# Kernel optimization log

Hardware: AMD Instinct MI355X
Metric: run time of the kernel (lower is better)

## Reference

```python
import jax, jax.numpy as jnp
import numpy as np

H = 32          # hidden_size
L = 10          # linear_size
EPS = 1e-14


def _lstm_cell(x, h, c, Wih, Whh, bih, bhh):
    # torch LSTMCell: gates ordered [i, f, g, o]
    gates = x @ Wih.T + bih + h @ Whh.T + bhh
    i, f, g, o = jnp.split(gates, 4, axis=-1)
    i = jax.nn.sigmoid(i)
    f = jax.nn.sigmoid(f)
    g = jnp.tanh(g)
    o = jax.nn.sigmoid(o)
    c_new = f * c + i * g
    h_new = o * jnp.tanh(c_new)
    return h_new, c_new


def setup_inputs() -> dict:
    key = jax.random.key(0)
    ks = jax.random.split(key, 24)
    B, N = 8, 100000
    inp = {
        "x": jax.random.normal(ks[0], (B, N), jnp.float32),
        "grad": jax.random.normal(ks[1], (B, N), jnp.float32),
        "h0": jax.random.normal(ks[2], (B, N, H), jnp.float32),
        "c0": jax.random.normal(ks[3], (B, N, H), jnp.float32),
        "h1": jax.random.normal(ks[4], (B, N, H), jnp.float32),
        "c1": jax.random.normal(ks[5], (B, N, H), jnp.float32),
        # initial_transform: Linear(2, L) -> tanh -> Linear(L, L)
        "W1": jax.random.normal(ks[6], (L, 2), jnp.float32) * 0.3,
        "b1": jax.random.normal(ks[7], (L,), jnp.float32) * 0.1,
        "W2": jax.random.normal(ks[8], (L, L), jnp.float32) * 0.3,
        "b2": jax.random.normal(ks[9], (L,), jnp.float32) * 0.1,
        # LSTMCell layer 0 (input L) and layer 1 (input H)
        "Wih0": jax.random.normal(ks[10], (4 * H, L), jnp.float32) * 0.1,
        "Whh0": jax.random.normal(ks[11], (4 * H, H), jnp.float32) * 0.1,
        "bih0": jax.random.normal(ks[12], (4 * H,), jnp.float32) * 0.1,
        "bhh0": jax.random.normal(ks[13], (4 * H,), jnp.float32) * 0.1,
        "Wih1": jax.random.normal(ks[14], (4 * H, H), jnp.float32) * 0.1,
        "Whh1": jax.random.normal(ks[15], (4 * H, H), jnp.float32) * 0.1,
        "bih1": jax.random.normal(ks[16], (4 * H,), jnp.float32) * 0.1,
        "bhh1": jax.random.normal(ks[17], (4 * H,), jnp.float32) * 0.1,
        # fc: Linear(H, 1)
        "Wfc": jax.random.normal(ks[18], (1, H), jnp.float32) * 0.1,
        "bfc": jax.random.normal(ks[19], (1,), jnp.float32) * 0.1,
    }
    return inp


def reference(x, grad, h0, c0, h1, c1, W1, b1, W2, b2,
              Wih0, Whh0, bih0, bhh0, Wih1, Whh1, bih1, bhh1, Wfc, bfc):
    B, N = x.shape
    BN = B * N
    g = grad.reshape(BN, 1)
    # gradient preprocessing: [sign, log(|g| + eps)]
    inp = jnp.concatenate([jnp.sign(g), jnp.log(jnp.abs(g) + EPS)], axis=1)  # (BN, 2)
    t = jnp.tanh(inp @ W1.T + b1) @ W2.T + b2                                # (BN, L)
    # batched across all n variables simultaneously (no cross-variable recurrence)
    h0n, c0n = _lstm_cell(t, h0.reshape(BN, H), c0.reshape(BN, H), Wih0, Whh0, bih0, bhh0)
    h1n, c1n = _lstm_cell(h0n, h1.reshape(BN, H), c1.reshape(BN, H), Wih1, Whh1, bih1, bhh1)
    delta = (h1n @ Wfc.T + bfc).reshape(B, N)
    x_new = x + delta
    return (x_new,
            h0n.reshape(B, N, H), c0n.reshape(B, N, H),
            h1n.reshape(B, N, H), c1n.reshape(B, N, H),
            delta)
```

## Files before the change

### kernel.cpp

```cpp
#include <hip/hip_runtime.h>


typedef __attribute__((ext_vector_type(8))) short bf16x8;
typedef __attribute__((ext_vector_type(4))) float f32x4;

#define HH 32
#define LL 10
#define NG 128

__device__ __forceinline__ short f2bf(float x) {
  __bf16 b = (__bf16)x;
  return __builtin_bit_cast(short, b);
}
__device__ __forceinline__ float fsig(float x) {
  return __builtin_amdgcn_rcpf(1.0f + __expf(-x));
}
__device__ __forceinline__ float ftanh(float x) {
  return fmaf(2.0f, __builtin_amdgcn_rcpf(1.0f + __expf(-2.0f * x)), -1.0f);
}

__global__ __launch_bounds__(256, 3) void l2o_fused(
    const float* __restrict__ x, const float* __restrict__ grad,
    const float* __restrict__ h0, const float* __restrict__ c0,
    const float* __restrict__ h1, const float* __restrict__ c1,
    const float* __restrict__ W1, const float* __restrict__ b1,
    const float* __restrict__ W2, const float* __restrict__ b2,
    const float* __restrict__ Wih0, const float* __restrict__ Whh0,
    const float* __restrict__ bih0, const float* __restrict__ bhh0,
    const float* __restrict__ Wih1, const float* __restrict__ Whh1,
    const float* __restrict__ bih1, const float* __restrict__ bhh1,
    const float* __restrict__ Wfc, const float* __restrict__ bfc,
    float* __restrict__ out, int BNi)
{
  const size_t BN = (size_t)BNi;
  float* __restrict__ xout  = out;
  float* __restrict__ h0out = out + BN;
  float* __restrict__ c0out = out + BN + BN * HH;
  float* __restrict__ h1out = out + BN + 2 * BN * HH;
  float* __restrict__ c1out = out + BN + 3 * BN * HH;
  float* __restrict__ dout  = out + BN + 4 * BN * HH;

  __shared__ __align__(16) short wih0L[2][NG][8];
  __shared__ __align__(16) short whh0L[4][NG][8];
  __shared__ __align__(16) short wih1L[4][NG][8];
  __shared__ __align__(16) short whh1L[4][NG][8];
  __shared__ __align__(16) short tsg0[4][64][8];
  __shared__ __align__(4)  short tsg1[4][64][2];
  __shared__ __align__(16) short hsg[4][4][16][8];

  const int tid = threadIdx.x;
  for (int idx = tid; idx < NG * HH; idx += 256) {
    int n = idx >> 5, k = idx & 31;
    whh0L[k >> 3][n][k & 7] = f2bf(Whh0[n * HH + k]);
    wih1L[k >> 3][n][k & 7] = f2bf(Wih1[n * HH + k]);
    whh1L[k >> 3][n][k & 7] = f2bf(Whh1[n * HH + k]);
  }
  for (int idx = tid; idx < NG * 16; idx += 256) {
    int n = idx >> 4, k = idx & 15;
    wih0L[k >> 3][n][k & 7] = (k < LL) ? f2bf(Wih0[n * LL + k]) : (short)0;
  }

  const int lane = tid & 63;
  const int w = tid >> 6;
  const int col = lane & 15;
  const int g = lane >> 4;

  float biasv0[8], biasv1[8];
#pragma unroll
  for (int nt = 0; nt < 8; ++nt) {
    biasv0[nt] = bih0[nt * 16 + col] + bhh0[nt * 16 + col];
    biasv1[nt] = bih1[nt * 16 + col] + bhh1[nt * 16 + col];
  }
  const float wfc0 = Wfc[col], wfc1 = Wfc[16 + col];
  const float bfcv = bfc[0];

  const int ebase = blockIdx.x * 256 + w * 64;

  {
    float gv = grad[ebase + lane];
    float sg = (gv > 0.f) ? 1.f : ((gv < 0.f) ? -1.f : 0.f);
    float lg = __logf(fabsf(gv) + 1e-14f);
    float u[LL], t[LL];
#pragma unroll
    for (int j = 0; j < LL; ++j)
      u[j] = ftanh(W1[2 * j] * sg + W1[2 * j + 1] * lg + b1[j]);
#pragma unroll
    for (int j = 0; j < LL; ++j) {
      float a = b2[j];
#pragma unroll
      for (int k = 0; k < LL; ++k) a += W2[j * LL + k] * u[k];
      t[j] = a;
    }
    bf16x8 tv0;
#pragma unroll
    for (int s = 0; s < 8; ++s) tv0[s] = f2bf(t[s]);
    *reinterpret_cast<bf16x8*>(&tsg0[w][lane][0]) = tv0;
    tsg1[w][lane][0] = f2bf(t[8]);
    tsg1[w][lane][1] = f2bf(t[9]);
  }
  __syncthreads();

#pragma unroll 1
  for (int st = 0; st < 4; ++st) {
    const int m16 = ebase + st * 16;
    const int mrow = 4 * g;

    bf16x8 a_t = {0, 0, 0, 0, 0, 0, 0, 0};
    if (g == 0) a_t = *reinterpret_cast<const bf16x8*>(&tsg0[w][st * 16 + col][0]);
    else if (g == 1) {
      a_t[0] = tsg1[w][st * 16 + col][0];
      a_t[1] = tsg1[w][st * 16 + col][1];
    }
    const float4* hp = reinterpret_cast<const float4*>(h0 + (size_t)(m16 + col) * HH + 8 * g);
    float4 v0 = hp[0], v1 = hp[1];
    bf16x8 a_h0;
    a_h0[0] = f2bf(v0.x); a_h0[1] = f2bf(v0.y); a_h0[2] = f2bf(v0.z); a_h0[3] = f2bf(v0.w);
    a_h0[4] = f2bf(v1.x); a_h0[5] = f2bf(v1.y); a_h0[6] = f2bf(v1.z); a_h0[7] = f2bf(v1.w);

    float c0r[2][4];
#pragma unroll
    for (int kk = 0; kk < 2; ++kk)
#pragma unroll
      for (int r = 0; r < 4; ++r)
        c0r[kk][r] = c0[(size_t)(m16 + mrow + r) * HH + kk * 16 + col];

    f32x4 acc[8];
#pragma unroll
    for (int nt = 0; nt < 8; ++nt) {
      float bv = biasv0[nt];
      f32x4 a = {bv, bv, bv, bv};
      acc[nt] = a;
    }
#pragma unroll
    for (int nt = 0; nt < 8; ++nt) {
      bf16x8 bih = {0, 0, 0, 0, 0, 0, 0, 0};
      if (g < 2) bih = *reinterpret_cast<const bf16x8*>(&wih0L[g][nt * 16 + col][0]);
      acc[nt] = __builtin_amdgcn_mfma_f32_16x16x32_bf16(a_t, bih, acc[nt], 0, 0, 0);
      bf16x8 bhh = *reinterpret_cast<const bf16x8*>(&whh0L[g][nt * 16 + col][0]);
      acc[nt] = __builtin_amdgcn_mfma_f32_16x16x32_bf16(a_h0, bhh, acc[nt], 0, 0, 0);
    }

    const float4* h1p = reinterpret_cast<const float4*>(h1 + (size_t)(m16 + col) * HH + 8 * g);
    float4 w0 = h1p[0], w1v = h1p[1];

#pragma unroll
    for (int kk = 0; kk < 2; ++kk) {
      const int k = kk * 16 + col;
#pragma unroll
      for (int r = 0; r < 4; ++r) {
        const size_t e2 = (size_t)(m16 + mrow + r);
        float iv = fsig(acc[0 + kk][r]);
        float fv = fsig(acc[2 + kk][r]);
        float gv = ftanh(acc[4 + kk][r]);
        float ov = fsig(acc[6 + kk][r]);
        float cn = fv * c0r[kk][r] + iv * gv;
        float hn = ov * ftanh(cn);
        c0out[e2 * HH + k] = cn;
        h0out[e2 * HH + k] = hn;
        hsg[w][k >> 3][mrow + r][k & 7] = f2bf(hn);
      }
    }
    asm volatile("s_waitcnt lgkmcnt(0)" ::: "memory");

    bf16x8 a_hn = *reinterpret_cast<const bf16x8*>(&hsg[w][g][col][0]);
    bf16x8 a_h1;
    a_h1[0] = f2bf(w0.x);  a_h1[1] = f2bf(w0.y);  a_h1[2] = f2bf(w0.z);  a_h1[3] = f2bf(w0.w);
    a_h1[4] = f2bf(w1v.x); a_h1[5] = f2bf(w1v.y); a_h1[6] = f2bf(w1v.z); a_h1[7] = f2bf(w1v.w);

    float c1r[2][4];
#pragma unroll
    for (int kk = 0; kk < 2; ++kk)
#pragma unroll
      for (int r = 0; r < 4; ++r)
        c1r[kk][r] = c1[(size_t)(m16 + mrow + r) * HH + kk * 16 + col];

#pragma unroll
    for (int nt = 0; nt < 8; ++nt) {
      float bv = biasv1[nt];
      f32x4 a = {bv, bv, bv, bv};
      acc[nt] = a;
    }
#pragma unroll
    for (int nt = 0; nt < 8; ++nt) {
      bf16x8 bih = *reinterpret_cast<const bf16x8*>(&wih1L[g][nt * 16 + col][0]);
      acc[nt] = __builtin_amdgcn_mfma_f32_16x16x32_bf16(a_hn, bih, acc[nt], 0, 0, 0);
      bf16x8 bhh = *reinterpret_cast<const bf16x8*>(&whh1L[g][nt * 16 + col][0]);
      acc[nt] = __builtin_amdgcn_mfma_f32_16x16x32_bf16(a_h1, bhh, acc[nt], 0, 0, 0);
    }

    float dsum[4] = {0.f, 0.f, 0.f, 0.f};
#pragma unroll
    for (int kk = 0; kk < 2; ++kk) {
      const int k = kk * 16 + col;
      const float wf = kk ? wfc1 : wfc0;
#pragma unroll
      for (int r = 0; r < 4; ++r) {
        const size_t e2 = (size_t)(m16 + mrow + r);
        float iv = fsig(acc[0 + kk][r]);
        float fv = fsig(acc[2 + kk][r]);
        float gv = ftanh(acc[4 + kk][r]);
        float ov = fsig(acc[6 + kk][r]);
        float cn = fv * c1r[kk][r] + iv * gv;
        float hn = ov * ftanh(cn);
        c1out[e2 * HH + k] = cn;
        h1out[e2 * HH + k] = hn;
        dsum[r] += hn * wf;
      }
    }
#pragma unroll
    for (int off = 1; off < 16; off <<= 1) {
#pragma unroll
      for (int r = 0; r < 4; ++r) dsum[r] += __shfl_xor(dsum[r], off, 64);
    }
    if (col == 0) {
      const int e4 = m16 + mrow;
      float4 xv = *reinterpret_cast<const float4*>(x + e4);
      float4 dv = {dsum[0] + bfcv, dsum[1] + bfcv, dsum[2] + bfcv, dsum[3] + bfcv};
      *reinterpret_cast<float4*>(dout + e4) = dv;
      float4 xn = {xv.x + dv.x, xv.y + dv.y, xv.z + dv.z, xv.w + dv.w};
      *reinterpret_cast<float4*>(xout + e4) = xn;
    }
  }
}

extern "C" void kernel_launch(void* const* d_in, const int* in_sizes, int n_in,
                              void* d_out, int out_size, void* d_ws, size_t ws_size,
                              hipStream_t stream) {
  const float* x    = (const float*)d_in[0];
  const float* grad = (const float*)d_in[1];
  const float* h0   = (const float*)d_in[2];
  const float* c0   = (const float*)d_in[3];
  const float* h1   = (const float*)d_in[4];
  const float* c1   = (const float*)d_in[5];
  const float* W1   = (const float*)d_in[6];
  const float* b1   = (const float*)d_in[7];
  const float* W2   = (const float*)d_in[8];
  const float* b2   = (const float*)d_in[9];
  const float* Wih0 = (const float*)d_in[10];
  const float* Whh0 = (const float*)d_in[11];
  const float* bih0 = (const float*)d_in[12];
  const float* bhh0 = (const float*)d_in[13];
  const float* Wih1 = (const float*)d_in[14];
  const float* Whh1 = (const float*)d_in[15];
  const float* bih1 = (const float*)d_in[16];
  const float* bhh1 = (const float*)d_in[17];
  const float* Wfc  = (const float*)d_in[18];
  const float* bfc  = (const float*)d_in[19];
  const int BN = in_sizes[0];
  const int nblk = BN / 256;
  l2o_fused<<<nblk, 256, 0, stream>>>(x, grad, h0, c0, h1, c1, W1, b1, W2, b2,
                                      Wih0, Whh0, bih0, bhh0, Wih1, Whh1,
                                      bih1, bhh1, Wfc, bfc, (float*)d_out, BN);
}
```

Measured before the change: 218.3 us.

## Software-pipeline per-subtile state loads with double-buffered register tiles

Gathers the h0/h1/c0/c1 loads for each 16-row subtile into a Tile struct and issues the next subtile's loads before computing the current one. The four-iteration loop becomes four unrolled calls that alternate two register buffers. This is meant to hide global memory latency behind the MFMA and activation work. It roughly doubles the live registers for the loaded state, which risks spills or lower occupancy under launch_bounds(256,3).

```diff
diff --git a/kernel.cpp b/kernel.cpp
--- a/kernel.cpp
+++ b/kernel.cpp
@@ -18,6 +18,13 @@
 __device__ __forceinline__ float ftanh(float x) {
   return fmaf(2.0f, __builtin_amdgcn_rcpf(1.0f + __expf(-2.0f * x)), -1.0f);
 }
+
+struct Tile {
+  float4 v0, v1;
+  float4 w0, w1;
+  float c0r[2][4];
+  float c1r[2][4];
+};
 
 __global__ __launch_bounds__(256, 3) void l2o_fused(
     const float* __restrict__ x, const float* __restrict__ grad,
@@ -64,6 +71,7 @@
   const int w = tid >> 6;
   const int col = lane & 15;
   const int g = lane >> 4;
+  const int mrow = 4 * g;
 
   float biasv0[8], biasv1[8];
 #pragma unroll
@@ -98,12 +106,26 @@
     tsg1[w][lane][0] = f2bf(t[8]);
     tsg1[w][lane][1] = f2bf(t[9]);
   }
-  __syncthreads();
-
-#pragma unroll 1
-  for (int st = 0; st < 4; ++st) {
+
+  auto load_tile = [&](Tile& T, int st) {
     const int m16 = ebase + st * 16;
-    const int mrow = 4 * g;
+    const float4* hp = reinterpret_cast<const float4*>(h0 + (size_t)(m16 + col) * HH + 8 * g);
+    T.v0 = hp[0]; T.v1 = hp[1];
+    const float4* h1p = reinterpret_cast<const float4*>(h1 + (size_t)(m16 + col) * HH + 8 * g);
+    T.w0 = h1p[0]; T.w1 = h1p[1];
+#pragma unroll
+    for (int kk = 0; kk < 2; ++kk)
+#pragma unroll
+      for (int r = 0; r < 4; ++r) {
+        T.c0r[kk][r] = c0[(size_t)(m16 + mrow + r) * HH + kk * 16 + col];
+        T.c1r[kk][r] = c1[(size_t)(m16 + mrow + r) * HH + kk * 16 + col];
+      }
+  };
+
+  auto body = [&](Tile& cur, Tile& nxt, const int st, const bool pf) {
+    const int m16 = ebase + st * 16;
+
+    if (pf) load_tile(nxt, st + 1);
 
     bf16x8 a_t = {0, 0, 0, 0, 0, 0, 0, 0};
     if (g == 0) a_t = *reinterpret_cast<const bf16x8*>(&tsg0[w][st * 16 + col][0]);
@@ -111,18 +133,9 @@
       a_t[0] = tsg1[w][st * 16 + col][0];
       a_t[1] = tsg1[w][st * 16 + col][1];
     }
-    const float4* hp = reinterpret_cast<const float4*>(h0 + (size_t)(m16 + col) * HH + 8 * g);
-    float4 v0 = hp[0], v1 = hp[1];
     bf16x8 a_h0;
-    a_h0[0] = f2bf(v0.x); a_h0[1] = f2bf(v0.y); a_h0[2] = f2bf(v0.z); a_h0[3] = f2bf(v0.w);
-    a_h0[4] = f2bf(v1.x); a_h0[5] = f2bf(v1.y); a_h0[6] = f2bf(v1.z); a_h0[7] = f2bf(v1.w);
-
-    float c0r[2][4];
-#pragma unroll
-    for (int kk = 0; kk < 2; ++kk)
-#pragma unroll
-      for (int r = 0; r < 4; ++r)
-        c0r[kk][r] = c0[(size_t)(m16 + mrow + r) * HH + kk * 16 + col];
+    a_h0[0] = f2bf(cur.v0.x); a_h0[1] = f2bf(cur.v0.y); a_h0[2] = f2bf(cur.v0.z); a_h0[3] = f2bf(cur.v0.w);
+    a_h0[4] = f2bf(cur.v1.x); a_h0[5] = f2bf(cur.v1.y); a_h0[6] = f2bf(cur.v1.z); a_h0[7] = f2bf(cur.v1.w);
 
     f32x4 acc[8];
 #pragma unroll
@@ -139,9 +152,6 @@
       bf16x8 bhh = *reinterpret_cast<const bf16x8*>(&whh0L[g][nt * 16 + col][0]);
       acc[nt] = __builtin_amdgcn_mfma_f32_16x16x32_bf16(a_h0, bhh, acc[nt], 0, 0, 0);
     }
-
-    const float4* h1p = reinterpret_cast<const float4*>(h1 + (size_t)(m16 + col) * HH + 8 * g);
-    float4 w0 = h1p[0], w1v = h1p[1];
 
 #pragma unroll
     for (int kk = 0; kk < 2; ++kk) {
@@ -153,7 +163,7 @@
         float fv = fsig(acc[2 + kk][r]);
         float gv = ftanh(acc[4 + kk][r]);
         float ov = fsig(acc[6 + kk][r]);
-        float cn = fv * c0r[kk][r] + iv * gv;
+        float cn = fv * cur.c0r[kk][r] + iv * gv;
         float hn = ov * ftanh(cn);
         c0out[e2 * HH + k] = cn;
         h0out[e2 * HH + k] = hn;
@@ -164,15 +174,8 @@
 
     bf16x8 a_hn = *reinterpret_cast<const bf16x8*>(&hsg[w][g][col][0]);
     bf16x8 a_h1;
-    a_h1[0] = f2bf(w0.x);  a_h1[1] = f2bf(w0.y);  a_h1[2] = f2bf(w0.z);  a_h1[3] = f2bf(w0.w);
-    a_h1[4] = f2bf(w1v.x); a_h1[5] = f2bf(w1v.y); a_h1[6] = f2bf(w1v.z); a_h1[7] = f2bf(w1v.w);
-
-    float c1r[2][4];
-#pragma unroll
-    for (int kk = 0; kk < 2; ++kk)
-#pragma unroll
-      for (int r = 0; r < 4; ++r)
-        c1r[kk][r] = c1[(size_t)(m16 + mrow + r) * HH + kk * 16 + col];
+    a_h1[0] = f2bf(cur.w0.x); a_h1[1] = f2bf(cur.w0.y); a_h1[2] = f2bf(cur.w0.z); a_h1[3] = f2bf(cur.w0.w);
+    a_h1[4] = f2bf(cur.w1.x); a_h1[5] = f2bf(cur.w1.y); a_h1[6] = f2bf(cur.w1.z); a_h1[7] = f2bf(cur.w1.w);
 
 #pragma unroll
     for (int nt = 0; nt < 8; ++nt) {
@@ -200,7 +203,7 @@
         float fv = fsig(acc[2 + kk][r]);
         float gv = ftanh(acc[4 + kk][r]);
         float ov = fsig(acc[6 + kk][r]);
-        float cn = fv * c1r[kk][r] + iv * gv;
+        float cn = fv * cur.c1r[kk][r] + iv * gv;
         float hn = ov * ftanh(cn);
         c1out[e2 * HH + k] = cn;
         h1out[e2 * HH + k] = hn;
@@ -220,7 +223,16 @@
       float4 xn = {xv.x + dv.x, xv.y + dv.y, xv.z + dv.z, xv.w + dv.w};
       *reinterpret_cast<float4*>(xout + e4) = xn;
     }
-  }
+  };
+
+  Tile T0, T1;
+  load_tile(T0, 0);
+  __syncthreads();
+
+  body(T0, T1, 0, true);
+  body(T1, T0, 1, true);
+  body(T0, T1, 2, true);
+  body(T1, T0, 3, false);
 }
 
 extern "C" void kernel_launch(void* const* d_in, const int* in_sizes, int n_in,
```

New measurement: 419.2 us. 92.1% more time.

## Double-buffer h/c state loads across sub-tiles and fully unroll step loop

Applied to the files above, without the earlier changes.

Prefetches h0, h1, c0 and c1 for the next 16-row sub-tile into a register double buffer while the current sub-tile runs its MFMAs and gate math. The first sub-tile's loads are issued before the shared-memory barrier. The step loop is now fully unrolled so the buffer indices resolve at compile time. The aim is to hide global load latency on this memory-bound kernel, at the cost of more VGPRs, which could cut occupancy under launch_bounds(256,3) or cause spills.

```diff
diff --git a/kernel.cpp b/kernel.cpp
--- a/kernel.cpp
+++ b/kernel.cpp
@@ -64,6 +64,7 @@
   const int w = tid >> 6;
   const int col = lane & 15;
   const int g = lane >> 4;
+  const int mrow = 4 * g;
 
   float biasv0[8], biasv1[8];
 #pragma unroll
@@ -98,12 +99,46 @@
     tsg1[w][lane][0] = f2bf(t[8]);
     tsg1[w][lane][1] = f2bf(t[9]);
   }
+
+  float4 pv0[2], pv1[2], pw0[2], pw1[2];
+  float  pc0[2][2][4], pc1[2][2][4];
+
+  {
+    const int m16 = ebase;
+    const float4* hp  = reinterpret_cast<const float4*>(h0 + (size_t)(m16 + col) * HH + 8 * g);
+    pv0[0] = hp[0]; pv1[0] = hp[1];
+    const float4* h1p = reinterpret_cast<const float4*>(h1 + (size_t)(m16 + col) * HH + 8 * g);
+    pw0[0] = h1p[0]; pw1[0] = h1p[1];
+#pragma unroll
+    for (int kk = 0; kk < 2; ++kk)
+#pragma unroll
+      for (int r = 0; r < 4; ++r) {
+        pc0[0][kk][r] = c0[(size_t)(m16 + mrow + r) * HH + kk * 16 + col];
+        pc1[0][kk][r] = c1[(size_t)(m16 + mrow + r) * HH + kk * 16 + col];
+      }
+  }
   __syncthreads();
 
-#pragma unroll 1
+#pragma unroll
   for (int st = 0; st < 4; ++st) {
+    const int cur = st & 1;
+    const int nx  = cur ^ 1;
     const int m16 = ebase + st * 16;
-    const int mrow = 4 * g;
+
+    if (st < 3) {
+      const int m16n = m16 + 16;
+      const float4* hp  = reinterpret_cast<const float4*>(h0 + (size_t)(m16n + col) * HH + 8 * g);
+      pv0[nx] = hp[0]; pv1[nx] = hp[1];
+      const float4* h1p = reinterpret_cast<const float4*>(h1 + (size_t)(m16n + col) * HH + 8 * g);
+      pw0[nx] = h1p[0]; pw1[nx] = h1p[1];
+#pragma unroll
+      for (int kk = 0; kk < 2; ++kk)
+#pragma unroll
+        for (int r = 0; r < 4; ++r) {
+          pc0[nx][kk][r] = c0[(size_t)(m16n + mrow + r) * HH + kk * 16 + col];
+          pc1[nx][kk][r] = c1[(size_t)(m16n + mrow + r) * HH + kk * 16 + col];
+        }
+    }
 
     bf16x8 a_t = {0, 0, 0, 0, 0, 0, 0, 0};
     if (g == 0) a_t = *reinterpret_cast<const bf16x8*>(&tsg0[w][st * 16 + col][0]);
@@ -111,18 +146,9 @@
       a_t[0] = tsg1[w][st * 16 + col][0];
       a_t[1] = tsg1[w][st * 16 + col][1];
     }
-    const float4* hp = reinterpret_cast<const float4*>(h0 + (size_t)(m16 + col) * HH + 8 * g);
-    float4 v0 = hp[0], v1 = hp[1];
     bf16x8 a_h0;
-    a_h0[0] = f2bf(v0.x); a_h0[1] = f2bf(v0.y); a_h0[2] = f2bf(v0.z); a_h0[3] = f2bf(v0.w);
-    a_h0[4] = f2bf(v1.x); a_h0[5] = f2bf(v1.y); a_h0[6] = f2bf(v1.z); a_h0[7] = f2bf(v1.w);
-
-    float c0r[2][4];
-#pragma unroll
-    for (int kk = 0; kk < 2; ++kk)
-#pragma unroll
-      for (int r = 0; r < 4; ++r)
-        c0r[kk][r] = c0[(size_t)(m16 + mrow + r) * HH + kk * 16 + col];
+    a_h0[0] = f2bf(pv0[cur].x); a_h0[1] = f2bf(pv0[cur].y); a_h0[2] = f2bf(pv0[cur].z); a_h0[3] = f2bf(pv0[cur].w);
+    a_h0[4] = f2bf(pv1[cur].x); a_h0[5] = f2bf(pv1[cur].y); a_h0[6] = f2bf(pv1[cur].z); a_h0[7] = f2bf(pv1[cur].w);
 
     f32x4 acc[8];
 #pragma unroll
@@ -139,9 +165,6 @@
       bf16x8 bhh = *reinterpret_cast<const bf16x8*>(&whh0L[g][nt * 16 + col][0]);
       acc[nt] = __builtin_amdgcn_mfma_f32_16x16x32_bf16(a_h0, bhh, acc[nt], 0, 0, 0);
     }
-
-    const float4* h1p = reinterpret_cast<const float4*>(h1 + (size_t)(m16 + col) * HH + 8 * g);
-    float4 w0 = h1p[0], w1v = h1p[1];
 
 #pragma unroll
     for (int kk = 0; kk < 2; ++kk) {
@@ -153,7 +176,7 @@
         float fv = fsig(acc[2 + kk][r]);
         float gv = ftanh(acc[4 + kk][r]);
         float ov = fsig(acc[6 + kk][r]);
-        float cn = fv * c0r[kk][r] + iv * gv;
+        float cn = fv * pc0[cur][kk][r] + iv * gv;
         float hn = ov * ftanh(cn);
         c0out[e2 * HH + k] = cn;
         h0out[e2 * HH + k] = hn;
@@ -164,15 +187,8 @@
 
     bf16x8 a_hn = *reinterpret_cast<const bf16x8*>(&hsg[w][g][col][0]);
     bf16x8 a_h1;
-    a_h1[0] = f2bf(w0.x);  a_h1[1] = f2bf(w0.y);  a_h1[2] = f2bf(w0.z);  a_h1[3] = f2bf(w0.w);
-    a_h1[4] = f2bf(w1v.x); a_h1[5] = f2bf(w1v.y); a_h1[6] = f2bf(w1v.z); a_h1[7] = f2bf(w1v.w);
-
-    float c1r[2][4];
-#pragma unroll
-    for (int kk = 0; kk < 2; ++kk)
-#pragma unroll
-      for (int r = 0; r < 4; ++r)
-        c1r[kk][r] = c1[(size_t)(m16 + mrow + r) * HH + kk * 16 + col];
+    a_h1[0] = f2bf(pw0[cur].x); a_h1[1] = f2bf(pw0[cur].y); a_h1[2] = f2bf(pw0[cur].z); a_h1[3] = f2bf(pw0[cur].w);
+    a_h1[4] = f2bf(pw1[cur].x); a_h1[5] = f2bf(pw1[cur].y); a_h1[6] = f2bf(pw1[cur].z); a_h1[7] = f2bf(pw1[cur].w);
 
 #pragma unroll
     for (int nt = 0; nt < 8; ++nt) {
@@ -200,7 +216,7 @@
         float fv = fsig(acc[2 + kk][r]);
         float gv = ftanh(acc[4 + kk][r]);
         float ov = fsig(acc[6 + kk][r]);
-        float cn = fv * c1r[kk][r] + iv * gv;
+        float cn = fv * pc1[cur][kk][r] + iv * gv;
         float hn = ov * ftanh(cn);
         c1out[e2 * HH + k] = cn;
         h1out[e2 * HH + k] = hn;
```

New measurement: 340.6 us. 56.0% more time.
